# Optimization experiments

Hardware: AMD Instinct MI355X
Metric: run time of the kernel (lower is better)

Reference implementation:

```python
import jax, jax.numpy as jnp
import numpy as np

M, TS, NX, NY = 24, 60, 192, 192   # solutions, source timesteps, source grid
H, D = 4, 8                         # num_heads, d_head
SIGMA = 0.2
N_TIME_STEPS = 50
T_MAX = 200.0
LX = 100.0                          # solutions[0]['params']['Lx']
SRC_T_MAX = 200.0                   # solutions[0]['params']['t_max']
NG = 50                             # target grid resolution (hard-coded in source)


def setup_inputs():
    key = jax.random.key(0)
    ks = jax.random.split(key, 8)
    c1_preds = jax.random.normal(ks[0], (M, TS, NX, NY), jnp.float32)
    c2_preds = jax.random.normal(ks[1], (M, TS, NX, NY), jnp.float32)
    lys = 30.0 + 90.0 * jax.random.uniform(ks[2], (M,), jnp.float32)
    c_cus = 0.0029 * jax.random.uniform(ks[3], (M,), jnp.float32)
    c_nis = 0.0018 * jax.random.uniform(ks[4], (M,), jnp.float32)
    params = jnp.stack([lys, c_cus, c_nis], axis=1)  # [M,3]
    # nonuniform, sorted per-solution y grid spanning [0, Ly_m]
    base = jnp.linspace(0.0, 1.0, NY, dtype=jnp.float32) ** 1.2
    src_y = lys[:, None] * base[None, :]  # [M,NY]
    src_t_last = 100.0 + 200.0 * jax.random.uniform(ks[5], (M,), jnp.float32)
    Wq = 0.3 * jax.random.normal(ks[6], (3, H * D), jnp.float32)
    Wk = 0.3 * jax.random.normal(ks[7], (3, H * D), jnp.float32)
    bq = jnp.zeros((H * D,), jnp.float32)
    bk = jnp.zeros((H * D,), jnp.float32)
    return dict(c1_preds=c1_preds, c2_preds=c2_preds, params=params, src_y=src_y,
                src_t_last=src_t_last, Wq=Wq, bq=bq, Wk=Wk, bk=bk,
                ly_target=jnp.float32(75.0), c_cu_target=jnp.float32(0.0015),
                c_ni_target=jnp.float32(0.0009))


def _axis_interp(grid, q):
    """1-D linear interp setup. grid [G] sorted, q [P] -> (idx, frac, in_bounds)."""
    G = grid.shape[-1]
    idx = jnp.clip(jnp.searchsorted(grid, q, side='right') - 1, 0, G - 2)
    g0 = jnp.take(grid, idx)
    g1 = jnp.take(grid, idx + 1)
    frac = (q - g0) / (g1 - g0)
    inb = (q >= grid[0]) & (q <= grid[-1])  # scipy fill_value=0 outside
    return idx, frac, inb


def reference(c1_preds, c2_preds, params, src_y, src_t_last, Wq, bq, Wk, bk,
              ly_target, c_cu_target, c_ni_target):
    lys, c_cus, c_nis = params[:, 0], params[:, 1], params[:, 2]
    # normalization exactly as in the torch forward
    ly_n = (lys - 30.0) / (120.0 - 30.0)
    cu_n = c_cus / 0.0029
    ni_n = c_nis / 0.0018
    t_ly = (ly_target - 30.0) / (120.0 - 30.0)
    t_cu = c_cu_target / 0.0029
    t_ni = c_ni_target / 0.0018

    p = jnp.stack([ly_n, cu_n, ni_n], axis=1)            # [M,3]
    tgt = jnp.stack([t_ly, t_cu, t_ni])[None, :]          # [1,3]
    Q = (tgt @ Wq + bq).reshape(H, D)                     # [H,D]
    K = (p @ Wk + bk).reshape(-1, H, D)                   # [M,H,D]
    logits = jnp.einsum('mhd,hd->mh', K, Q) / jnp.sqrt(jnp.float32(D))
    attn = jax.nn.softmax(logits, axis=0).mean(axis=1)    # softmax over solutions, mean heads -> [M]

    dist2 = ((ly_n - t_ly) ** 2 + (cu_n - t_cu) ** 2 + (ni_n - t_ni) ** 2) / SIGMA ** 2
    sw = jnp.exp(-dist2 / 2.0)
    sw = sw / (sw.sum() + 1e-12)
    w = attn * sw
    w = w / (w.sum() + 1e-12)
    w = jax.lax.stop_gradient(w)  # original detaches weights before interpolation

    # ---- physics-aware interpolation ----
    times = jnp.linspace(0.0, min(SRC_T_MAX, T_MAX), N_TIME_STEPS)  # [T]
    ti = jnp.clip(jnp.round(times[:, None] / src_t_last[None, :] * (TS - 1)).astype(jnp.int32),
                  0, TS - 1)                                         # [T,M]

    src_x = jnp.linspace(0.0, LX, NX)
    qx = jnp.linspace(0.0, LX, NG)
    qy = (jnp.arange(NG, dtype=jnp.float32) / (NG - 1)) * ly_target  # linspace(0, ly_target, NG)

    ix, fx, mx = _axis_interp(src_x, qx)                             # [NG] each (shared x grid)
    scale = ly_target / lys                                           # [M]
    y_scaled = src_y * scale[:, None]                                 # [M,NY]
    iy, fy, my = jax.vmap(lambda g: _axis_interp(g, qy))(y_scaled)    # [M,NG] each
    mask = (mx[None, :, None] & my[:, None, :]).astype(c1_preds.dtype)  # [M,NG,NG]

    T = N_TIME_STEPS
    iy_b = jnp.broadcast_to(iy[None, :, None, :], (T, M, NG, NG))
    iy1_b = jnp.broadcast_to((iy + 1)[None, :, None, :], (T, M, NG, NG))

    def interp_field(preds):
        vals = preds[jnp.arange(M)[None, :], ti]                      # [T,M,NX,NY] time gather
        fxc = fx[None, None, :, None]
        vx = vals[:, :, ix, :] * (1.0 - fxc) + vals[:, :, ix + 1, :] * fxc  # [T,M,NG,NY]
        v0 = jnp.take_along_axis(vx, iy_b, axis=3)                    # [T,M,NG,NG]
        v1 = jnp.take_along_axis(vx, iy1_b, axis=3)
        fyc = fy[None, :, None, :]
        v = (v0 * (1.0 - fyc) + v1 * fyc) * mask[None]
        return jnp.einsum('tmij,m->tij', v, w)                        # weighted sum over solutions

    c1 = interp_field(c1_preds).at[:, :, 0].set(c_cu_target)
    c2 = interp_field(c2_preds).at[:, :, -1].set(c_ni_target)
    return jnp.stack([c1, c2])  # [2, T, NG, NG]
```

## Files before the change

kernel.cpp:

```cpp
#include <hip/hip_runtime.h>
#include <math.h>

#define M   24
#define TS  60
#define NX  192
#define NY  192
#define H_  4
#define D_  8
#define NTS 50
#define NG  50

__device__ float g_w[M];
__device__ int   g_ti[NTS][M];
__device__ int   g_ix[NG];
__device__ float g_fx[NG];
__device__ float g_mx[NG];
__device__ int   g_iy[M][NG];
__device__ float g_fy[M][NG];
__device__ float g_my[M][NG];

__global__ __launch_bounds__(256) void prep_kernel(
    const float* __restrict__ params, const float* __restrict__ src_y,
    const float* __restrict__ stl,
    const float* __restrict__ Wq, const float* __restrict__ bq,
    const float* __restrict__ Wk, const float* __restrict__ bk,
    const float* __restrict__ lyt_p, const float* __restrict__ ccu_p,
    const float* __restrict__ cni_p)
{
    const int tid = threadIdx.x;
    __shared__ float s_logits[M][H_];
    __shared__ float s_sw[M];

    const float ly_target = lyt_p[0];
    const float c_cu_t = ccu_p[0];
    const float c_ni_t = cni_p[0];

    const float t_ly = (ly_target - 30.0f) / 90.0f;
    const float t_cu = c_cu_t / 0.0029f;
    const float t_ni = c_ni_t / 0.0018f;

    if (tid < M) {
        const int m = tid;
        const float ly  = params[m*3 + 0];
        const float ccu = params[m*3 + 1];
        const float cni = params[m*3 + 2];
        const float ly_n = (ly - 30.0f) / 90.0f;
        const float cu_n = ccu / 0.0029f;
        const float ni_n = cni / 0.0018f;
        for (int h = 0; h < H_; ++h) {
            float acc = 0.0f;
            for (int d = 0; d < D_; ++d) {
                const int col = h*D_ + d;
                const float q = t_ly*Wq[0*32+col] + t_cu*Wq[1*32+col] + t_ni*Wq[2*32+col] + bq[col];
                const float k = ly_n*Wk[0*32+col] + cu_n*Wk[1*32+col] + ni_n*Wk[2*32+col] + bk[col];
                acc += k * q;
            }
            s_logits[m][h] = acc / sqrtf(8.0f);
        }
        const float dly = ly_n - t_ly, dcu = cu_n - t_cu, dni = ni_n - t_ni;
        const float d2 = (dly*dly + dcu*dcu + dni*dni) / 0.04f;
        s_sw[m] = expf(-d2 * 0.5f);
    }
    __syncthreads();

    if (tid == 0) {
        float attn[M];
        for (int m = 0; m < M; ++m) attn[m] = 0.0f;
        for (int h = 0; h < H_; ++h) {
            float mxv = -1e30f;
            for (int m = 0; m < M; ++m) mxv = fmaxf(mxv, s_logits[m][h]);
            float e[M]; float s = 0.0f;
            for (int m = 0; m < M; ++m) { e[m] = expf(s_logits[m][h] - mxv); s += e[m]; }
            for (int m = 0; m < M; ++m) attn[m] += e[m] / s;
        }
        float ssw = 0.0f;
        for (int m = 0; m < M; ++m) ssw += s_sw[m];
        float w[M]; float wsum = 0.0f;
        for (int m = 0; m < M; ++m) {
            w[m] = (attn[m] * 0.25f) * (s_sw[m] / (ssw + 1e-12f));
            wsum += w[m];
        }
        for (int m = 0; m < M; ++m) g_w[m] = w[m] / (wsum + 1e-12f);
    }

    const float step_t = 200.0f / 49.0f;
    for (int idx = tid; idx < NTS*M; idx += blockDim.x) {
        const int t = idx / M, m = idx % M;
        const float tt = (t == NTS-1) ? 200.0f : step_t * (float)t;
        const float r = tt / stl[m] * 59.0f;
        int ti = (int)rintf(r);
        ti = ti < 0 ? 0 : (ti > TS-1 ? TS-1 : ti);
        g_ti[t][m] = ti;
    }

    if (tid < NG) {
        const int i = tid;
        const float step_x = 100.0f / 191.0f;
        const float step_q = 100.0f / 49.0f;
        const float q = (i == NG-1) ? 100.0f : step_q * (float)i;
        int pos = 0;
        for (int g = 0; g < NX; ++g) {
            const float gv = (g == NX-1) ? 100.0f : step_x * (float)g;
            if (gv <= q) pos = g + 1;
        }
        int id = pos - 1;
        id = id < 0 ? 0 : (id > NX-2 ? NX-2 : id);
        const float g0 = (id   == NX-1) ? 100.0f : step_x * (float)id;
        const float g1 = (id+1 == NX-1) ? 100.0f : step_x * (float)(id+1);
        g_ix[i] = id;
        g_fx[i] = (q - g0) / (g1 - g0);
        g_mx[i] = (q >= 0.0f && q <= 100.0f) ? 1.0f : 0.0f;
    }

    for (int idx = tid; idx < M*NG; idx += blockDim.x) {
        const int m = idx / NG, j = idx % NG;
        const float scale = ly_target / params[m*3 + 0];
        const float q = (float)j / 49.0f * ly_target;
        const float* sy = src_y + m*NY;
        int pos = 0;
        for (int g = 0; g < NY; ++g) {
            const float gv = sy[g] * scale;
            if (gv <= q) pos = g + 1;
        }
        int id = pos - 1;
        id = id < 0 ? 0 : (id > NY-2 ? NY-2 : id);
        const float g0 = sy[id] * scale;
        const float g1 = sy[id+1] * scale;
        g_iy[m][j] = id;
        g_fy[m][j] = (q - g0) / (g1 - g0);
        const float gfirst = sy[0] * scale;
        const float glast  = sy[NY-1] * scale;
        g_my[m][j] = (q >= gfirst && q <= glast) ? 1.0f : 0.0f;
    }
}

__global__ __launch_bounds__(256) void interp_kernel(
    const float* __restrict__ c1, const float* __restrict__ c2,
    float* __restrict__ out,
    const float* __restrict__ ccu_p, const float* __restrict__ cni_p)
{
    const int p = blockIdx.x * blockDim.x + threadIdx.x;
    if (p >= NG*NG) return;
    const int t = blockIdx.y;
    const int f = blockIdx.z;
    const int i = p / NG;
    const int j = p % NG;

    const float* __restrict__ preds = (f == 0) ? c1 : c2;

    const int   ixi = g_ix[i];
    const float fxi = g_fx[i];
    const float mxi = g_mx[i];

    float acc = 0.0f;
    #pragma unroll 4
    for (int m = 0; m < M; ++m) {
        const int tim   = g_ti[t][m];
        const int iyj   = g_iy[m][j];
        const float fyj = g_fy[m][j];
        const float msk = mxi * g_my[m][j];
        const float wm  = g_w[m];
        const float* base = preds + (((size_t)m*TS + tim)*NX + ixi)*(size_t)NY + iyj;
        const float v00 = base[0];
        const float v01 = base[1];
        const float v10 = base[NY];
        const float v11 = base[NY + 1];
        const float vx0 = v00*(1.0f - fxi) + v10*fxi;
        const float vx1 = v01*(1.0f - fxi) + v11*fxi;
        const float v   = (vx0*(1.0f - fyj) + vx1*fyj) * msk;
        acc += v * wm;
    }

    if (f == 0 && j == 0)    acc = ccu_p[0];
    if (f == 1 && j == NG-1) acc = cni_p[0];

    out[(((size_t)f*NTS + t)*NG + i)*NG + j] = acc;
}

extern "C" void kernel_launch(void* const* d_in, const int* in_sizes, int n_in,
                              void* d_out, int out_size, void* d_ws, size_t ws_size,
                              hipStream_t stream) {
    const float* c1     = (const float*)d_in[0];
    const float* c2     = (const float*)d_in[1];
    const float* params = (const float*)d_in[2];
    const float* src_y  = (const float*)d_in[3];
    const float* stl    = (const float*)d_in[4];
    const float* Wq     = (const float*)d_in[5];
    const float* bq     = (const float*)d_in[6];
    const float* Wk     = (const float*)d_in[7];
    const float* bk     = (const float*)d_in[8];
    const float* lyt    = (const float*)d_in[9];
    const float* ccut   = (const float*)d_in[10];
    const float* cnit   = (const float*)d_in[11];
    float* out = (float*)d_out;

    prep_kernel<<<1, 256, 0, stream>>>(params, src_y, stl, Wq, bq, Wk, bk, lyt, ccut, cnit);

    dim3 grid((NG*NG + 255) / 256, NTS, 2);
    interp_kernel<<<grid, 256, 0, stream>>>(c1, c2, out, ccut, cnit);
}
```

Measured before the change: 411.5 us.

## Fuse both fields per thread, stage per-m tables in LDS, binary-search prep

The interp kernel now handles both c1 and c2 in one thread, sharing the offset, weight and fraction math, and halves the grid's z dimension. Per-solution tables (time offsets, weights, y indices, fractions, masks) are staged into shared memory per block. The prep kernel replaces its linear grid scans with binary searches and parallelises the per-head softmax across threads. In exchange, each block pays a table-staging cost, launches half as many blocks, and holds more registers per thread.

```diff
diff --git a/kernel.cpp b/kernel.cpp
--- a/kernel.cpp
+++ b/kernel.cpp
@@ -30,14 +30,13 @@
     const int tid = threadIdx.x;
     __shared__ float s_logits[M][H_];
     __shared__ float s_sw[M];
+    __shared__ float s_eh[H_][M];
 
     const float ly_target = lyt_p[0];
-    const float c_cu_t = ccu_p[0];
-    const float c_ni_t = cni_p[0];
 
     const float t_ly = (ly_target - 30.0f) / 90.0f;
-    const float t_cu = c_cu_t / 0.0029f;
-    const float t_ni = c_ni_t / 0.0018f;
+    const float t_cu = ccu_p[0] / 0.0029f;
+    const float t_ni = cni_p[0] / 0.0018f;
 
     if (tid < M) {
         const int m = tid;
@@ -63,21 +62,24 @@
     }
     __syncthreads();
 
+    if (tid < H_) {
+        const int h = tid;
+        float mxv = -1e30f;
+        for (int m = 0; m < M; ++m) mxv = fmaxf(mxv, s_logits[m][h]);
+        float e[M]; float s = 0.0f;
+        for (int m = 0; m < M; ++m) { e[m] = expf(s_logits[m][h] - mxv); s += e[m]; }
+        for (int m = 0; m < M; ++m) s_eh[h][m] = e[m] / s;
+    }
+    __syncthreads();
+
     if (tid == 0) {
-        float attn[M];
-        for (int m = 0; m < M; ++m) attn[m] = 0.0f;
-        for (int h = 0; h < H_; ++h) {
-            float mxv = -1e30f;
-            for (int m = 0; m < M; ++m) mxv = fmaxf(mxv, s_logits[m][h]);
-            float e[M]; float s = 0.0f;
-            for (int m = 0; m < M; ++m) { e[m] = expf(s_logits[m][h] - mxv); s += e[m]; }
-            for (int m = 0; m < M; ++m) attn[m] += e[m] / s;
-        }
         float ssw = 0.0f;
         for (int m = 0; m < M; ++m) ssw += s_sw[m];
         float w[M]; float wsum = 0.0f;
         for (int m = 0; m < M; ++m) {
-            w[m] = (attn[m] * 0.25f) * (s_sw[m] / (ssw + 1e-12f));
+            float attn = 0.0f;
+            for (int h = 0; h < H_; ++h) attn += s_eh[h][m];
+            w[m] = (attn * 0.25f) * (s_sw[m] / (ssw + 1e-12f));
             wsum += w[m];
         }
         for (int m = 0; m < M; ++m) g_w[m] = w[m] / (wsum + 1e-12f);
@@ -98,12 +100,13 @@
         const float step_x = 100.0f / 191.0f;
         const float step_q = 100.0f / 49.0f;
         const float q = (i == NG-1) ? 100.0f : step_q * (float)i;
-        int pos = 0;
-        for (int g = 0; g < NX; ++g) {
-            const float gv = (g == NX-1) ? 100.0f : step_x * (float)g;
-            if (gv <= q) pos = g + 1;
-        }
-        int id = pos - 1;
+        int lo = 0, hi = NX;
+        while (lo < hi) {
+            const int mid = (lo + hi) >> 1;
+            const float gv = (mid == NX-1) ? 100.0f : step_x * (float)mid;
+            if (gv <= q) lo = mid + 1; else hi = mid;
+        }
+        int id = lo - 1;
         id = id < 0 ? 0 : (id > NX-2 ? NX-2 : id);
         const float g0 = (id   == NX-1) ? 100.0f : step_x * (float)id;
         const float g1 = (id+1 == NX-1) ? 100.0f : step_x * (float)(id+1);
@@ -117,12 +120,13 @@
         const float scale = ly_target / params[m*3 + 0];
         const float q = (float)j / 49.0f * ly_target;
         const float* sy = src_y + m*NY;
-        int pos = 0;
-        for (int g = 0; g < NY; ++g) {
-            const float gv = sy[g] * scale;
-            if (gv <= q) pos = g + 1;
-        }
-        int id = pos - 1;
+        int lo = 0, hi = NY;
+        while (lo < hi) {
+            const int mid = (lo + hi) >> 1;
+            const float gv = sy[mid] * scale;
+            if (gv <= q) lo = mid + 1; else hi = mid;
+        }
+        int id = lo - 1;
         id = id < 0 ? 0 : (id > NY-2 ? NY-2 : id);
         const float g0 = sy[id] * scale;
         const float g1 = sy[id+1] * scale;
@@ -139,42 +143,73 @@
     float* __restrict__ out,
     const float* __restrict__ ccu_p, const float* __restrict__ cni_p)
 {
-    const int p = blockIdx.x * blockDim.x + threadIdx.x;
+    const int t   = blockIdx.y;
+    const int tid = threadIdx.x;
+
+    __shared__ int   s_off[M];
+    __shared__ float s_w[M];
+    __shared__ int   s_iy[M][NG];
+    __shared__ float s_fy[M][NG];
+    __shared__ float s_my[M][NG];
+
+    if (tid < M) {
+        s_off[tid] = (tid*TS + g_ti[t][tid]) * (NX*NY);
+        s_w[tid]   = g_w[tid];
+    }
+    for (int idx = tid; idx < M*NG; idx += 256) {
+        const int m = idx / NG, j = idx % NG;
+        s_iy[m][j] = g_iy[m][j];
+        s_fy[m][j] = g_fy[m][j];
+        s_my[m][j] = g_my[m][j];
+    }
+    __syncthreads();
+
+    const int p = blockIdx.x * 256 + tid;
     if (p >= NG*NG) return;
-    const int t = blockIdx.y;
-    const int f = blockIdx.z;
     const int i = p / NG;
     const int j = p % NG;
 
-    const float* __restrict__ preds = (f == 0) ? c1 : c2;
-
-    const int   ixi = g_ix[i];
-    const float fxi = g_fx[i];
-    const float mxi = g_mx[i];
-
-    float acc = 0.0f;
-    #pragma unroll 4
+    const int   ixNY = g_ix[i] * NY;
+    const float fxi  = g_fx[i];
+    const float mxi  = g_mx[i];
+
+    float acc0 = 0.0f;
+    float acc1 = 0.0f;
+    #pragma unroll 8
     for (int m = 0; m < M; ++m) {
-        const int tim   = g_ti[t][m];
-        const int iyj   = g_iy[m][j];
-        const float fyj = g_fy[m][j];
-        const float msk = mxi * g_my[m][j];
-        const float wm  = g_w[m];
-        const float* base = preds + (((size_t)m*TS + tim)*NX + ixi)*(size_t)NY + iyj;
-        const float v00 = base[0];
-        const float v01 = base[1];
-        const float v10 = base[NY];
-        const float v11 = base[NY + 1];
-        const float vx0 = v00*(1.0f - fxi) + v10*fxi;
-        const float vx1 = v01*(1.0f - fxi) + v11*fxi;
-        const float v   = (vx0*(1.0f - fyj) + vx1*fyj) * msk;
-        acc += v * wm;
-    }
-
-    if (f == 0 && j == 0)    acc = ccu_p[0];
-    if (f == 1 && j == NG-1) acc = cni_p[0];
-
-    out[(((size_t)f*NTS + t)*NG + i)*NG + j] = acc;
+        const int   off = s_off[m] + ixNY + s_iy[m][j];
+        const float fyj = s_fy[m][j];
+        const float msk = mxi * s_my[m][j];
+        const float wm  = s_w[m];
+
+        const float* __restrict__ b1 = c1 + off;
+        const float* __restrict__ b2 = c2 + off;
+
+        const float a00 = b1[0];
+        const float a01 = b1[1];
+        const float a10 = b1[NY];
+        const float a11 = b1[NY + 1];
+        const float b00 = b2[0];
+        const float b01 = b2[1];
+        const float b10 = b2[NY];
+        const float b11 = b2[NY + 1];
+
+        const float ax0 = a00*(1.0f - fxi) + a10*fxi;
+        const float ax1 = a01*(1.0f - fxi) + a11*fxi;
+        const float av  = (ax0*(1.0f - fyj) + ax1*fyj) * msk;
+        acc0 += av * wm;
+
+        const float bx0 = b00*(1.0f - fxi) + b10*fxi;
+        const float bx1 = b01*(1.0f - fxi) + b11*fxi;
+        const float bv  = (bx0*(1.0f - fyj) + bx1*fyj) * msk;
+        acc1 += bv * wm;
+    }
+
+    if (j == 0)      acc0 = ccu_p[0];
+    if (j == NG-1)   acc1 = cni_p[0];
+
+    out[(((size_t)0*NTS + t)*NG + i)*NG + j] = acc0;
+    out[(((size_t)1*NTS + t)*NG + i)*NG + j] = acc1;
 }
 
 extern "C" void kernel_launch(void* const* d_in, const int* in_sizes, int n_in,
@@ -196,6 +231,6 @@
 
     prep_kernel<<<1, 256, 0, stream>>>(params, src_y, stl, Wq, bq, Wk, bk, lyt, ccut, cnit);
 
-    dim3 grid((NG*NG + 255) / 256, NTS, 2);
+    dim3 grid((NG*NG + 255) / 256, NTS, 1);
     interp_kernel<<<grid, 256, 0, stream>>>(c1, c2, out, ccut, cnit);
 }
```

Result: faster. 400.4 us (-2.7%).
